# Kernel tuning notes

Hardware: AMD Instinct MI355X
Metric: run time of the kernel (lower is better)

Reference implementation:

```python
import jax, jax.numpy as jnp
import numpy as np

GH, GW, B, H, OUT = 9, 9, 1024, 256, 1


def setup_inputs() -> dict:
    key = jax.random.key(0)
    ks = jax.random.split(key, 16)
    N = GH * GW
    s3 = 1.0 / np.sqrt(3 * H)
    sH = 1.0 / np.sqrt(H)
    return {
        "x": jax.random.normal(ks[0], (B, GH, GW), jnp.float32),
        "h_ext": jax.random.normal(ks[1], (B, H), jnp.float32),
        "c_ext": jax.random.normal(ks[2], (B, H), jnp.float32),
        "grid_h": jax.random.normal(ks[3], (GH, GW, B, H), jnp.float32),
        "grid_c": jax.random.normal(ks[4], (GH, GW, B, H), jnp.float32),
        "W_hp": jax.random.normal(ks[5], (N, H, 3 * H), jnp.float32) * s3,
        "b_hp": jax.random.normal(ks[6], (N, H), jnp.float32) * s3,
        "W_cp": jax.random.normal(ks[7], (N, H, 3 * H), jnp.float32) * s3,
        "b_cp": jax.random.normal(ks[8], (N, H), jnp.float32) * s3,
        "W_ih": jax.random.normal(ks[9], (N, 4 * H, 1), jnp.float32) * sH,
        "W_hh": jax.random.normal(ks[10], (N, 4 * H, H), jnp.float32) * sH,
        "b_ih": jax.random.normal(ks[11], (N, 4 * H), jnp.float32) * sH,
        "b_hh": jax.random.normal(ks[12], (N, 4 * H), jnp.float32) * sH,
        "W_out": jax.random.normal(ks[13], (OUT, H), jnp.float32) * sH,
        "b_out": jnp.zeros((OUT,), jnp.float32),
    }


def _lstm_cell(x_cell, h0, c0, W_ih_k, W_hh_k, b_ih_k, b_hh_k):
    # x_cell: [B,1], h0/c0: [B,H]; torch LSTMCell math
    gates = x_cell @ W_ih_k.T + b_ih_k + h0 @ W_hh_k.T + b_hh_k  # [B,4H]
    i, f, g, o = jnp.split(gates, 4, axis=1)
    i, f, o = jax.nn.sigmoid(i), jax.nn.sigmoid(f), jax.nn.sigmoid(o)
    g = jnp.tanh(g)
    c = f * c0 + i * g
    h = o * jnp.tanh(c)
    return h, c


def reference(x, h_ext, c_ext, grid_h, grid_c,
              W_hp, b_hp, W_cp, b_cp,
              W_ih, W_hh, b_ih, b_hh, W_out, b_out):
    zeros = jnp.zeros((B, H), x.dtype)
    # new states, updated in raster order; left/up neighbors read NEW states
    new_h = [[None] * GW for _ in range(GH)]
    new_c = [[None] * GW for _ in range(GH)]
    for i in range(GH):
        for j in range(GW):
            k = i * GW + j
            h_prev, c_prev = grid_h[i, j], grid_c[i, j]
            if i == 0 and j == 0:
                h_left, c_left = h_ext, c_ext
            elif j > 0:
                h_left, c_left = new_h[i][j - 1], new_c[i][j - 1]
            else:
                h_left, c_left = zeros, zeros
            if i > 0:
                h_up, c_up = new_h[i - 1][j], new_c[i - 1][j]
            else:
                h_up, c_up = zeros, zeros
            comb_h = jnp.concatenate([h_left, h_up, h_prev], axis=1)  # [B,3H]
            comb_c = jnp.concatenate([c_left, c_up, c_prev], axis=1)
            ph = comb_h @ W_hp[k].T + b_hp[k]
            pc = comb_c @ W_cp[k].T + b_cp[k]
            x_cell = x[:, i, j][:, None]  # [B,1]
            h_new, c_new = _lstm_cell(x_cell, ph, pc, W_ih[k], W_hh[k], b_ih[k], b_hh[k])
            new_h[i][j], new_c[i][j] = h_new, c_new
    final_h, final_c = new_h[-1][-1], new_c[-1][-1]
    # fc_out with fc_layers_out=[0]: Linear + ReLU, then sigmoid
    out = jax.nn.sigmoid(jax.nn.relu(final_h @ W_out.T + b_out))
    gh = jnp.stack([jnp.stack(r, 0) for r in new_h], 0)
    gc = jnp.stack([jnp.stack(r, 0) for r in new_c], 0)
    return out, final_h, final_c, gh, gc
```

## Files before the change

### kernel.cpp

```cpp
#include <hip/hip_runtime.h>
#include <math.h>

#define BATCH 1024
#define HID 256

typedef __bf16 bf16_t;
typedef __bf16 bf16x8 __attribute__((ext_vector_type(8)));
typedef float f32x4 __attribute__((ext_vector_type(4)));

struct ProjDesc {
    const float* left;
    const float* up;
    const float* prev;
    const float* W;
    const float* bias;
    float* out;
};
struct ProjBatchArgs { ProjDesc d[18]; };

struct CellDesc {
    const float* ph;
    const float* pc;
    const float* Whh;
    const float* Wih;
    const float* bih;
    const float* bhh;
    const float* xcol;
    float* gh;
    float* gc;
};
struct CellBatchArgs { CellDesc d[9]; };

__device__ inline bf16x8 cvt8(const float4 a, const float4 b) {
    bf16x8 r;
    r[0] = (bf16_t)a.x; r[1] = (bf16_t)a.y; r[2] = (bf16_t)a.z; r[3] = (bf16_t)a.w;
    r[4] = (bf16_t)b.x; r[5] = (bf16_t)b.y; r[6] = (bf16_t)b.z; r[7] = (bf16_t)b.w;
    return r;
}

__global__ __launch_bounds__(256) void proj_kernel(ProjBatchArgs args) {
    const ProjDesc pd = args.d[blockIdx.z];
    __shared__ bf16_t Asm[64][40];
    __shared__ bf16_t Bsm[128][40];
    const int t = threadIdx.x;
    const int lane = t & 63, wid = t >> 6;
    const int wm = wid & 1, wn = wid >> 1;
    const int ln = lane & 15, lh = lane >> 4;
    const int b0 = blockIdx.x * 64;
    const int n0 = blockIdx.y * 128;
    const int lr_a = t >> 2, lq_a = (t & 3) * 8;
    const int lr_b = t >> 1, lq_b = (t & 1) * 16;

    f32x4 acc[2][4] = {};
    const float* wrow = pd.W + (size_t)(n0 + lr_b) * (3 * HID) + lq_b;
    const float* srcs[3] = { pd.left, pd.up, pd.prev };

    for (int seg = 0; seg < 3; ++seg) {
        const float* sp = srcs[seg];
        if (!sp) continue;
        const float* arow = sp + (size_t)(b0 + lr_a) * HID + lq_a;
        const float* wseg = wrow + seg * HID;
        for (int kb = 0; kb < 8; ++kb) {
            const float4 a0 = *(const float4*)(arow + kb * 32);
            const float4 a1 = *(const float4*)(arow + kb * 32 + 4);
            const float4 w0 = *(const float4*)(wseg + kb * 32);
            const float4 w1 = *(const float4*)(wseg + kb * 32 + 4);
            const float4 w2 = *(const float4*)(wseg + kb * 32 + 8);
            const float4 w3 = *(const float4*)(wseg + kb * 32 + 12);
            const bf16x8 av  = cvt8(a0, a1);
            const bf16x8 bv0 = cvt8(w0, w1);
            const bf16x8 bv1 = cvt8(w2, w3);
            __syncthreads();
            *(bf16x8*)&Asm[lr_a][lq_a] = av;
            *(bf16x8*)&Bsm[lr_b][lq_b] = bv0;
            *(bf16x8*)&Bsm[lr_b][lq_b + 8] = bv1;
            __syncthreads();
            bf16x8 af[2], bfr[4];
            #pragma unroll
            for (int mf = 0; mf < 2; ++mf)
                af[mf] = *(const bf16x8*)&Asm[wm * 32 + mf * 16 + ln][lh * 8];
            #pragma unroll
            for (int nf = 0; nf < 4; ++nf)
                bfr[nf] = *(const bf16x8*)&Bsm[wn * 64 + nf * 16 + ln][lh * 8];
            #pragma unroll
            for (int mf = 0; mf < 2; ++mf)
                #pragma unroll
                for (int nf = 0; nf < 4; ++nf)
                    acc[mf][nf] = __builtin_amdgcn_mfma_f32_16x16x32_bf16(
                        af[mf], bfr[nf], acc[mf][nf], 0, 0, 0);
        }
    }
    #pragma unroll
    for (int nf = 0; nf < 4; ++nf) {
        const int n = n0 + wn * 64 + nf * 16 + ln;
        const float bias = pd.bias[n];
        #pragma unroll
        for (int mf = 0; mf < 2; ++mf)
            #pragma unroll
            for (int r = 0; r < 4; ++r) {
                const int b = b0 + wm * 32 + mf * 16 + lh * 4 + r;
                pd.out[(size_t)b * HID + n] = acc[mf][nf][r] + bias;
            }
    }
}

__global__ __launch_bounds__(256) void cell_kernel(CellBatchArgs args) {
    const CellDesc cd = args.d[blockIdx.z];
    __shared__ bf16_t Psm[128][40];
    __shared__ bf16_t Wsm[128][40];
    const int t = threadIdx.x;
    const int lane = t & 63, wid = t >> 6;
    const int wm = wid & 1, wn = wid >> 1;
    const int ln = lane & 15, lh = lane >> 4;
    const int b0 = blockIdx.x * 128;
    const int u0 = blockIdx.y * 32;
    const int lr = t >> 1, lq = (t & 1) * 16;

    f32x4 acc[4][4] = {};
    const float* prow = cd.ph + (size_t)(b0 + lr) * HID + lq;
    const int cg = lr >> 5, cdu = lr & 31;
    const float* wrow = cd.Whh + (size_t)(cg * HID + u0 + cdu) * HID + lq;

    for (int kb = 0; kb < 8; ++kb) {
        const float4 p0 = *(const float4*)(prow + kb * 32);
        const float4 p1 = *(const float4*)(prow + kb * 32 + 4);
        const float4 p2 = *(const float4*)(prow + kb * 32 + 8);
        const float4 p3 = *(const float4*)(prow + kb * 32 + 12);
        const float4 w0 = *(const float4*)(wrow + kb * 32);
        const float4 w1 = *(const float4*)(wrow + kb * 32 + 4);
        const float4 w2 = *(const float4*)(wrow + kb * 32 + 8);
        const float4 w3 = *(const float4*)(wrow + kb * 32 + 12);
        const bf16x8 pv0 = cvt8(p0, p1), pv1 = cvt8(p2, p3);
        const bf16x8 wv0 = cvt8(w0, w1), wv1 = cvt8(w2, w3);
        __syncthreads();
        *(bf16x8*)&Psm[lr][lq] = pv0;
        *(bf16x8*)&Psm[lr][lq + 8] = pv1;
        *(bf16x8*)&Wsm[lr][lq] = wv0;
        *(bf16x8*)&Wsm[lr][lq + 8] = wv1;
        __syncthreads();
        bf16x8 af[4], bfr[4];
        #pragma unroll
        for (int mf = 0; mf < 4; ++mf)
            af[mf] = *(const bf16x8*)&Psm[wm * 64 + mf * 16 + ln][lh * 8];
        #pragma unroll
        for (int g = 0; g < 4; ++g)
            bfr[g] = *(const bf16x8*)&Wsm[g * 32 + wn * 16 + ln][lh * 8];
        #pragma unroll
        for (int mf = 0; mf < 4; ++mf)
            #pragma unroll
            for (int g = 0; g < 4; ++g)
                acc[mf][g] = __builtin_amdgcn_mfma_f32_16x16x32_bf16(
                    af[mf], bfr[g], acc[mf][g], 0, 0, 0);
    }

    const int u = u0 + wn * 16 + ln;
    float wih[4], bsum[4];
    #pragma unroll
    for (int g = 0; g < 4; ++g) {
        const int n = g * HID + u;
        wih[g] = cd.Wih[n];
        bsum[g] = cd.bih[n] + cd.bhh[n];
    }
    #pragma unroll
    for (int mf = 0; mf < 4; ++mf)
        #pragma unroll
        for (int r = 0; r < 4; ++r) {
            const int b = b0 + wm * 64 + mf * 16 + lh * 4 + r;
            const float xv = cd.xcol[(size_t)b * 81];
            const float gi = acc[mf][0][r] + xv * wih[0] + bsum[0];
            const float gf = acc[mf][1][r] + xv * wih[1] + bsum[1];
            const float gg = acc[mf][2][r] + xv * wih[2] + bsum[2];
            const float go = acc[mf][3][r] + xv * wih[3] + bsum[3];
            const float i_ = 1.f / (1.f + expf(-gi));
            const float f_ = 1.f / (1.f + expf(-gf));
            const float o_ = 1.f / (1.f + expf(-go));
            const float g_ = tanhf(gg);
            const float c0 = cd.pc[(size_t)b * HID + u];
            const float cn = f_ * c0 + i_ * g_;
            const float hn = o_ * tanhf(cn);
            cd.gh[(size_t)b * HID + u] = hn;
            cd.gc[(size_t)b * HID + u] = cn;
        }
}

__global__ __launch_bounds__(256) void final_kernel(
        const float* __restrict__ gh88, const float* __restrict__ gc88,
        const float* __restrict__ Wout, const float* __restrict__ bout,
        float* __restrict__ out, float* __restrict__ fh, float* __restrict__ fc) {
    const int tid = blockIdx.x * blockDim.x + threadIdx.x;
    const int nth = gridDim.x * blockDim.x;
    for (int idx = tid; idx < BATCH * HID; idx += nth) {
        fh[idx] = gh88[idx];
        fc[idx] = gc88[idx];
    }
    if (tid < BATCH) {
        float s = bout[0];
        for (int k = 0; k < HID; ++k) s += gh88[(size_t)tid * HID + k] * Wout[k];
        s = fmaxf(s, 0.f);
        out[tid] = 1.f / (1.f + expf(-s));
    }
}

extern "C" void kernel_launch(void* const* d_in, const int* in_sizes, int n_in,
                              void* d_out, int out_size, void* d_ws, size_t ws_size,
                              hipStream_t stream) {
    const float* x      = (const float*)d_in[0];
    const float* h_ext  = (const float*)d_in[1];
    const float* c_ext  = (const float*)d_in[2];
    const float* grid_h = (const float*)d_in[3];
    const float* grid_c = (const float*)d_in[4];
    const float* W_hp   = (const float*)d_in[5];
    const float* b_hp   = (const float*)d_in[6];
    const float* W_cp   = (const float*)d_in[7];
    const float* b_cp   = (const float*)d_in[8];
    const float* W_ih   = (const float*)d_in[9];
    const float* W_hh   = (const float*)d_in[10];
    const float* b_ih   = (const float*)d_in[11];
    const float* b_hh   = (const float*)d_in[12];
    const float* W_out  = (const float*)d_in[13];
    const float* b_out  = (const float*)d_in[14];

    float* out = (float*)d_out;
    float* fh  = out + BATCH * 1;
    float* fc  = fh + BATCH * HID;
    float* gh  = fc + BATCH * HID;
    float* gc  = gh + (size_t)81 * BATCH * HID;

    float* ws = (float*)d_ws;

    for (int d = 0; d <= 16; ++d) {
        const int i_lo = d > 8 ? d - 8 : 0;
        const int i_hi = d < 8 ? d : 8;
        const int nc = i_hi - i_lo + 1;
        ProjBatchArgs pa{};
        CellBatchArgs ca{};
        for (int s = 0; s < nc; ++s) {
            const int i = i_lo + s, j = d - i;
            const int k = i * 9 + j;
            const float *hl, *cl, *hu, *cu;
            if (i == 0 && j == 0)      { hl = h_ext; cl = c_ext; }
            else if (j > 0)            { hl = gh + (size_t)(k - 1) * BATCH * HID;
                                         cl = gc + (size_t)(k - 1) * BATCH * HID; }
            else                       { hl = nullptr; cl = nullptr; }
            if (i > 0)                 { hu = gh + (size_t)(k - 9) * BATCH * HID;
                                         cu = gc + (size_t)(k - 9) * BATCH * HID; }
            else                       { hu = nullptr; cu = nullptr; }
            const float* hp = grid_h + (size_t)k * BATCH * HID;
            const float* cp = grid_c + (size_t)k * BATCH * HID;
            float* ph = ws + (size_t)s * 2 * BATCH * HID;
            float* pc = ph + BATCH * HID;
            pa.d[2 * s + 0] = { hl, hu, hp, W_hp + (size_t)k * HID * 3 * HID,
                                b_hp + (size_t)k * HID, ph };
            pa.d[2 * s + 1] = { cl, cu, cp, W_cp + (size_t)k * HID * 3 * HID,
                                b_cp + (size_t)k * HID, pc };
            ca.d[s] = { ph, pc,
                        W_hh + (size_t)k * 4 * HID * HID,
                        W_ih + (size_t)k * 4 * HID,
                        b_ih + (size_t)k * 4 * HID,
                        b_hh + (size_t)k * 4 * HID,
                        x + i * 9 + j,
                        gh + (size_t)k * BATCH * HID,
                        gc + (size_t)k * BATCH * HID };
        }
        proj_kernel<<<dim3(16, 2, 2 * nc), 256, 0, stream>>>(pa);
        cell_kernel<<<dim3(8, 8, nc), 256, 0, stream>>>(ca);
    }
    final_kernel<<<dim3(64), 256, 0, stream>>>(
        gh + (size_t)80 * BATCH * HID, gc + (size_t)80 * BATCH * HID,
        W_out, b_out, out, fh, fc);
}
```

Measured before the change: 1.081 ms.

## Prefetch next K-tile into registers and enlarge proj tile to 128 rows

```diff
diff --git a/kernel.cpp b/kernel.cpp
--- a/kernel.cpp
+++ b/kernel.cpp
@@ -40,65 +40,76 @@
 
 __global__ __launch_bounds__(256) void proj_kernel(ProjBatchArgs args) {
     const ProjDesc pd = args.d[blockIdx.z];
-    __shared__ bf16_t Asm[64][40];
+    __shared__ bf16_t Asm[128][40];
     __shared__ bf16_t Bsm[128][40];
     const int t = threadIdx.x;
     const int lane = t & 63, wid = t >> 6;
     const int wm = wid & 1, wn = wid >> 1;
     const int ln = lane & 15, lh = lane >> 4;
-    const int b0 = blockIdx.x * 64;
+    const int b0 = blockIdx.x * 128;
     const int n0 = blockIdx.y * 128;
-    const int lr_a = t >> 2, lq_a = (t & 3) * 8;
-    const int lr_b = t >> 1, lq_b = (t & 1) * 16;
-
-    f32x4 acc[2][4] = {};
-    const float* wrow = pd.W + (size_t)(n0 + lr_b) * (3 * HID) + lq_b;
-    const float* srcs[3] = { pd.left, pd.up, pd.prev };
-
-    for (int seg = 0; seg < 3; ++seg) {
-        const float* sp = srcs[seg];
-        if (!sp) continue;
-        const float* arow = sp + (size_t)(b0 + lr_a) * HID + lq_a;
-        const float* wseg = wrow + seg * HID;
-        for (int kb = 0; kb < 8; ++kb) {
-            const float4 a0 = *(const float4*)(arow + kb * 32);
-            const float4 a1 = *(const float4*)(arow + kb * 32 + 4);
-            const float4 w0 = *(const float4*)(wseg + kb * 32);
-            const float4 w1 = *(const float4*)(wseg + kb * 32 + 4);
-            const float4 w2 = *(const float4*)(wseg + kb * 32 + 8);
-            const float4 w3 = *(const float4*)(wseg + kb * 32 + 12);
-            const bf16x8 av  = cvt8(a0, a1);
-            const bf16x8 bv0 = cvt8(w0, w1);
-            const bf16x8 bv1 = cvt8(w2, w3);
-            __syncthreads();
-            *(bf16x8*)&Asm[lr_a][lq_a] = av;
-            *(bf16x8*)&Bsm[lr_b][lq_b] = bv0;
-            *(bf16x8*)&Bsm[lr_b][lq_b + 8] = bv1;
-            __syncthreads();
-            bf16x8 af[2], bfr[4];
-            #pragma unroll
-            for (int mf = 0; mf < 2; ++mf)
-                af[mf] = *(const bf16x8*)&Asm[wm * 32 + mf * 16 + ln][lh * 8];
+    const int sr = t >> 1, sq = (t & 1) * 16;
+
+    const float* aSeg[3]; int kOff[3]; int nseg = 0;
+    if (pd.left) { aSeg[nseg] = pd.left; kOff[nseg] = 0;   ++nseg; }
+    if (pd.up)   { aSeg[nseg] = pd.up;   kOff[nseg] = 256; ++nseg; }
+    aSeg[nseg] = pd.prev; kOff[nseg] = 512; ++nseg;
+    const int iters = nseg * 8;
+
+    const size_t aoff = (size_t)(b0 + sr) * HID + sq;
+    const float* wbase = pd.W + (size_t)(n0 + sr) * (3 * HID) + sq;
+
+    f32x4 acc[4][4] = {};
+    float4 sa[4], sb[4];
+    {
+        const float* ap = aSeg[0] + aoff;
+        const float* wp = wbase + kOff[0];
+        #pragma unroll
+        for (int m = 0; m < 4; ++m) sa[m] = *(const float4*)(ap + m * 4);
+        #pragma unroll
+        for (int m = 0; m < 4; ++m) sb[m] = *(const float4*)(wp + m * 4);
+    }
+    for (int i = 0; i < iters; ++i) {
+        const bf16x8 av0 = cvt8(sa[0], sa[1]), av1 = cvt8(sa[2], sa[3]);
+        const bf16x8 bv0 = cvt8(sb[0], sb[1]), bv1 = cvt8(sb[2], sb[3]);
+        __syncthreads();
+        *(bf16x8*)&Asm[sr][sq] = av0;
+        *(bf16x8*)&Asm[sr][sq + 8] = av1;
+        *(bf16x8*)&Bsm[sr][sq] = bv0;
+        *(bf16x8*)&Bsm[sr][sq + 8] = bv1;
+        __syncthreads();
+        if (i + 1 < iters) {
+            const int s = (i + 1) >> 3, kb = (i + 1) & 7;
+            const float* ap = aSeg[s] + aoff + kb * 32;
+            const float* wp = wbase + kOff[s] + kb * 32;
+            #pragma unroll
+            for (int m = 0; m < 4; ++m) sa[m] = *(const float4*)(ap + m * 4);
+            #pragma unroll
+            for (int m = 0; m < 4; ++m) sb[m] = *(const float4*)(wp + m * 4);
+        }
+        bf16x8 af[4], bfv[4];
+        #pragma unroll
+        for (int mf = 0; mf < 4; ++mf)
+            af[mf] = *(const bf16x8*)&Asm[wm * 64 + mf * 16 + ln][lh * 8];
+        #pragma unroll
+        for (int nf = 0; nf < 4; ++nf)
+            bfv[nf] = *(const bf16x8*)&Bsm[wn * 64 + nf * 16 + ln][lh * 8];
+        #pragma unroll
+        for (int mf = 0; mf < 4; ++mf)
             #pragma unroll
             for (int nf = 0; nf < 4; ++nf)
-                bfr[nf] = *(const bf16x8*)&Bsm[wn * 64 + nf * 16 + ln][lh * 8];
-            #pragma unroll
-            for (int mf = 0; mf < 2; ++mf)
-                #pragma unroll
-                for (int nf = 0; nf < 4; ++nf)
-                    acc[mf][nf] = __builtin_amdgcn_mfma_f32_16x16x32_bf16(
-                        af[mf], bfr[nf], acc[mf][nf], 0, 0, 0);
-        }
+                acc[mf][nf] = __builtin_amdgcn_mfma_f32_16x16x32_bf16(
+                    af[mf], bfv[nf], acc[mf][nf], 0, 0, 0);
     }
     #pragma unroll
     for (int nf = 0; nf < 4; ++nf) {
         const int n = n0 + wn * 64 + nf * 16 + ln;
         const float bias = pd.bias[n];
         #pragma unroll
-        for (int mf = 0; mf < 2; ++mf)
+        for (int mf = 0; mf < 4; ++mf)
             #pragma unroll
             for (int r = 0; r < 4; ++r) {
-                const int b = b0 + wm * 32 + mf * 16 + lh * 4 + r;
+                const int b = b0 + wm * 64 + mf * 16 + lh * 4 + r;
                 pd.out[(size_t)b * HID + n] = acc[mf][nf][r] + bias;
             }
     }
@@ -114,30 +125,34 @@
     const int ln = lane & 15, lh = lane >> 4;
     const int b0 = blockIdx.x * 128;
     const int u0 = blockIdx.y * 32;
-    const int lr = t >> 1, lq = (t & 1) * 16;
+    const int sr = t >> 1, sq = (t & 1) * 16;
+
+    const float* pbase = cd.ph + (size_t)(b0 + sr) * HID + sq;
+    const int cg = sr >> 5, cdu = sr & 31;
+    const float* wbase = cd.Whh + (size_t)(cg * HID + u0 + cdu) * HID + sq;
 
     f32x4 acc[4][4] = {};
-    const float* prow = cd.ph + (size_t)(b0 + lr) * HID + lq;
-    const int cg = lr >> 5, cdu = lr & 31;
-    const float* wrow = cd.Whh + (size_t)(cg * HID + u0 + cdu) * HID + lq;
+    float4 sa[4], sb[4];
+    #pragma unroll
+    for (int m = 0; m < 4; ++m) sa[m] = *(const float4*)(pbase + m * 4);
+    #pragma unroll
+    for (int m = 0; m < 4; ++m) sb[m] = *(const float4*)(wbase + m * 4);
 
     for (int kb = 0; kb < 8; ++kb) {
-        const float4 p0 = *(const float4*)(prow + kb * 32);
-        const float4 p1 = *(const float4*)(prow + kb * 32 + 4);
-        const float4 p2 = *(const float4*)(prow + kb * 32 + 8);
-        const float4 p3 = *(const float4*)(prow + kb * 32 + 12);
-        const float4 w0 = *(const float4*)(wrow + kb * 32);
-        const float4 w1 = *(const float4*)(wrow + kb * 32 + 4);
-        const float4 w2 = *(const float4*)(wrow + kb * 32 + 8);
-        const float4 w3 = *(const float4*)(wrow + kb * 32 + 12);
-        const bf16x8 pv0 = cvt8(p0, p1), pv1 = cvt8(p2, p3);
-        const bf16x8 wv0 = cvt8(w0, w1), wv1 = cvt8(w2, w3);
-        __syncthreads();
-        *(bf16x8*)&Psm[lr][lq] = pv0;
-        *(bf16x8*)&Psm[lr][lq + 8] = pv1;
-        *(bf16x8*)&Wsm[lr][lq] = wv0;
-        *(bf16x8*)&Wsm[lr][lq + 8] = wv1;
-        __syncthreads();
+        const bf16x8 pv0 = cvt8(sa[0], sa[1]), pv1 = cvt8(sa[2], sa[3]);
+        const bf16x8 wv0 = cvt8(sb[0], sb[1]), wv1 = cvt8(sb[2], sb[3]);
+        __syncthreads();
+        *(bf16x8*)&Psm[sr][sq] = pv0;
+        *(bf16x8*)&Psm[sr][sq + 8] = pv1;
+        *(bf16x8*)&Wsm[sr][sq] = wv0;
+        *(bf16x8*)&Wsm[sr][sq + 8] = wv1;
+        __syncthreads();
+        if (kb + 1 < 8) {
+            #pragma unroll
+            for (int m = 0; m < 4; ++m) sa[m] = *(const float4*)(pbase + (kb + 1) * 32 + m * 4);
+            #pragma unroll
+            for (int m = 0; m < 4; ++m) sb[m] = *(const float4*)(wbase + (kb + 1) * 32 + m * 4);
+        }
         bf16x8 af[4], bfr[4];
         #pragma unroll
         for (int mf = 0; mf < 4; ++mf)
@@ -262,7 +277,7 @@
                         gh + (size_t)k * BATCH * HID,
                         gc + (size_t)k * BATCH * HID };
         }
-        proj_kernel<<<dim3(16, 2, 2 * nc), 256, 0, stream>>>(pa);
+        proj_kernel<<<dim3(8, 2, 2 * nc), 256, 0, stream>>>(pa);
         cell_kernel<<<dim3(8, 8, nc), 256, 0, stream>>>(ca);
     }
     final_kernel<<<dim3(64), 256, 0, stream>>>(
```

After: 1.151 ms. 6.5% more time.
